# Optimization experiments

Measured on AMD Instinct MI355X. Metric: run time of the kernel, lower is better.

The kernel has to match this reference:

```python
import jax, jax.numpy as jnp
import numpy as np
from jax import lax

T, N, H, A = 128, 64, 1024, 16  # timesteps, batch(envs), hidden_size, num_actions


def _ortho(key, shape):
    # approximate nn.init.orthogonal_ via QR of a gaussian
    a = jax.random.normal(key, shape, dtype=jnp.float32)
    flip = shape[0] < shape[1]
    q, r = jnp.linalg.qr(a.T if flip else a)
    q = q * jnp.sign(jnp.diagonal(r))
    return (q.T if flip else q).astype(jnp.float32)


def setup_inputs() -> dict:
    key = jax.random.key(0)
    ks = jax.random.split(key, 10)
    c = jax.random.normal(ks[0], (T * N, H), dtype=jnp.float32)
    hxs = jax.random.normal(ks[1], (N, 2 * H), dtype=jnp.float32)
    masks = jnp.ones((T * N, 1), dtype=jnp.float32)
    prev_action_one_hot = jax.random.uniform(ks[2], (T * N, A), dtype=jnp.float32)
    # GRUCell params (torch layout: weight_ih [3H, in], weight_hh [3H, H])
    w_ih_h = _ortho(ks[3], (3 * H, H))
    w_hh_h = _ortho(ks[4], (3 * H, H))
    b_ih_h = jnp.zeros((3 * H,), dtype=jnp.float32)
    b_hh_h = jnp.zeros((3 * H,), dtype=jnp.float32)
    w_ih_p = _ortho(ks[5], (3 * H, H))
    w_hh_p = _ortho(ks[6], (3 * H, H))
    b_ih_p = jnp.zeros((3 * H,), dtype=jnp.float32)
    b_hh_p = jnp.zeros((3 * H,), dtype=jnp.float32)
    # p_network: Linear(H+A, H) -> tanh -> Linear(H, A)
    p_w1 = jax.random.normal(ks[7], (H, H + A), dtype=jnp.float32) / np.sqrt(H + A)
    p_b1 = jnp.zeros((H,), dtype=jnp.float32)
    p_w2 = jax.random.normal(ks[8], (A, H), dtype=jnp.float32) / np.sqrt(H)
    p_b2 = jnp.zeros((A,), dtype=jnp.float32)
    return dict(c=c, hxs=hxs, masks=masks, prev_action_one_hot=prev_action_one_hot,
                w_ih_h=w_ih_h, w_hh_h=w_hh_h, b_ih_h=b_ih_h, b_hh_h=b_hh_h,
                w_ih_p=w_ih_p, w_hh_p=w_hh_p, b_ih_p=b_ih_p, b_hh_p=b_hh_p,
                p_w1=p_w1, p_b1=p_b1, p_w2=p_w2, p_b2=p_b2)


def _gru_cell(x, h, w_ih, w_hh, b_ih, b_hh):
    # torch.nn.GRUCell semantics
    gi = x @ w_ih.T + b_ih  # [N, 3H]
    gh = h @ w_hh.T + b_hh  # [N, 3H]
    i_r, i_z, i_n = jnp.split(gi, 3, axis=1)
    h_r, h_z, h_n = jnp.split(gh, 3, axis=1)
    r = jax.nn.sigmoid(i_r + h_r)
    z = jax.nn.sigmoid(i_z + h_z)
    n = jnp.tanh(i_n + r * h_n)
    return (1.0 - z) * n + z * h


def reference(c, hxs, masks, prev_action_one_hot,
              w_ih_h, w_hh_h, b_ih_h, b_hh_h,
              w_ih_p, w_hh_p, b_ih_p, b_hh_p,
              p_w1, p_b1, p_w2, p_b2):
    c3 = c.reshape(T, N, H)
    m3 = masks.reshape(T, N, 1)
    a3 = prev_action_one_hot.reshape(T, N, A)
    h0 = hxs[:, :H]
    pol0 = hxs[:, H:]

    def step(carry, xs):
        h, pol = carry
        c_t, m_t, a_t = xs
        p_in = jnp.concatenate([h, a_t], axis=1) * m_t
        p_dist = jnp.tanh(p_in @ p_w1.T + p_b1) @ p_w2.T + p_b2  # [N, A]
        h = _gru_cell(c_t, h * m_t, w_ih_h, w_hh_h, b_ih_h, b_hh_h)
        pol = _gru_cell(c_t, pol * m_t, w_ih_p, w_hh_p, b_ih_p, b_hh_p)
        return (h, pol), (p_dist, pol)

    (h, pol), (acc_p_dist, acc_policy) = lax.scan(step, (h0, pol0), (c3, m3, a3))
    acc_p_dist = acc_p_dist.reshape(T * N, -1)
    acc_policy = acc_policy.reshape(T * N, -1)
    hxs_out = jnp.concatenate([h, pol], axis=1)
    return acc_p_dist, acc_policy, hxs_out
```

## Files before the change

kernel.cpp:

```cpp
#include <hip/hip_runtime.h>
#include <hip/hip_bf16.h>
#include <math.h>

#define TT 128
#define NN 64
#define HH 1024
#define AA 16
#define G3 3072
#define NC 6144
#define PK 1088
#define WLDS_STRIDE 1032
#define GISL 3072

#define PD_OFF  0
#define POL_OFF (TT*NN*AA)
#define HXS_OFF (POL_OFF + TT*NN*HH)

typedef __attribute__((ext_vector_type(8))) short short8;
typedef __attribute__((ext_vector_type(4))) float f32x4;

__device__ __align__(16) __hip_bfloat16 g_c_bf[TT*NN*HH];
__device__ __align__(16) __hip_bfloat16 g_wihc_bf[NC*HH];
__device__ __align__(16) __hip_bfloat16 g_pw1_bf[HH*PK];
__device__ __align__(16) __hip_bfloat16 g_pw2_bf[AA*HH];
__device__ float g_gi2[(size_t)2*64*TT*GISL];
__device__ float g_h[NN*HH];
__device__ float g_pol[NN*HH];
__device__ __align__(16) __hip_bfloat16 g_pin_all[(size_t)(TT+1)*NN*PK];
__device__ __align__(16) __hip_bfloat16 g_polm_all[(size_t)(TT+1)*NN*HH];
__device__ __align__(16) __hip_bfloat16 g_ph_all[TT*NN*HH];

__device__ __align__(256) unsigned g_flagsA[2][64];
__device__ __align__(256) unsigned g_gi_cnt[64];
__device__ __align__(256) unsigned g_pol_cnt[64];

__device__ __forceinline__ float sigmoidf_(float x) { return 1.0f / (1.0f + __expf(-x)); }
__device__ __forceinline__ float tanhf_(float x) {
  float e = __expf(2.0f * x);
  return 1.0f - 2.0f / (e + 1.0f);
}

__global__ __launch_bounds__(256) void conv_all(
    const float* __restrict__ c, const float* __restrict__ masks, const float* __restrict__ act,
    const float* __restrict__ wih_h, const float* __restrict__ wih_p,
    const float* __restrict__ pw1, const float* __restrict__ pw2)
{
  size_t i = (size_t)blockIdx.x * 256 + threadIdx.x;
  size_t stride = (size_t)gridDim.x * 256;
  for (size_t f = i; f < (size_t)TT*NN*HH; f += stride) g_c_bf[f] = __float2bfloat16(c[f]);
  for (size_t f = i; f < (size_t)G3*HH; f += stride) {
    g_wihc_bf[f]                 = __float2bfloat16(wih_h[f]);
    g_wihc_bf[(size_t)G3*HH + f] = __float2bfloat16(wih_p[f]);
  }
  for (size_t f = i; f < (size_t)HH*PK; f += stride) {
    int o = (int)(f / PK), j = (int)(f % PK);
    g_pw1_bf[f] = (j < HH + AA) ? __float2bfloat16(pw1[(size_t)o*(HH+AA) + j]) : __float2bfloat16(0.0f);
  }
  for (size_t f = i; f < (size_t)AA*HH; f += stride) g_pw2_bf[f] = __float2bfloat16(pw2[f]);
  for (size_t f = i; f < (size_t)TT*NN*(PK-HH); f += stride) {
    int row = (int)(f >> 6), j = (int)(f & 63);
    float v = (j < AA) ? act[(size_t)row*AA + j] * masks[row] : 0.0f;
    g_pin_all[(size_t)row*PK + HH + j] = __float2bfloat16(v);
  }
}

__global__ __launch_bounds__(256) void init_kernel(const float* __restrict__ hxs,
                                                   const float* __restrict__ masks) {
  int f = blockIdx.x * 256 + threadIdx.x;
  int n = f >> 10, j = f & 1023;
  float m0 = masks[n];
  float hv = hxs[n * 2 * HH + j];
  float pv = hxs[n * 2 * HH + HH + j];
  g_h[f] = hv;
  g_pol[f] = pv;
  g_pin_all[(size_t)n * PK + j]  = __float2bfloat16(hv * m0);
  g_polm_all[(size_t)n * HH + j] = __float2bfloat16(pv * m0);
  if (f < 128)
    __hip_atomic_store(&g_flagsA[f >> 6][f & 63], 0u,
                       __ATOMIC_RELAXED, __HIP_MEMORY_SCOPE_AGENT);
  if (f >= 128 && f < 192)
    __hip_atomic_store(&g_gi_cnt[f - 128], 0u,
                       __ATOMIC_RELAXED, __HIP_MEMORY_SCOPE_AGENT);
  if (f >= 192 && f < 256)
    __hip_atomic_store(&g_pol_cnt[f - 192], 0u,
                       __ATOMIC_RELAXED, __HIP_MEMORY_SCOPE_AGENT);
}

__global__ __launch_bounds__(256, 1) void fused_scan(
    const float* __restrict__ masks,
    const float* __restrict__ whh_h, const float* __restrict__ whh_p,
    const float* __restrict__ bih_h, const float* __restrict__ bhh_h,
    const float* __restrict__ bih_p, const float* __restrict__ bhh_p,
    const float* __restrict__ pb1, const float* __restrict__ pb2,
    float* __restrict__ out)
{
  extern __shared__ __align__(16) __hip_bfloat16 Dyn[];
  __shared__ float m_lds[TT * NN];
  __shared__ __align__(8) __hip_bfloat16 sL[NN * 16];
  const int tid = threadIdx.x, l = tid & 63, w = tid >> 6;

  if (blockIdx.x < 128) {
    __hip_bfloat16* Ws = Dyn;
    const int gru = blockIdx.x >> 6;
    const int idx = blockIdx.x & 63;
    const int c0  = idx * 16;
    const float* __restrict__ Wf = (gru == 0) ? whh_h : whh_p;

    for (int i = tid; i < TT * NN; i += 256) m_lds[i] = masks[i];

    for (int ch = tid; ch < 48 * 128; ch += 256) {
      int row = ch >> 7, ko = (ch & 127) * 8;
      int gate = row >> 4, j = row & 15;
      const float* s = Wf + (size_t)(gate * HH + c0 + j) * HH + ko;
      union { short8 v; __hip_bfloat16 hh[8]; } tmp;
#pragma unroll
      for (int q = 0; q < 8; ++q) tmp.hh[q] = __float2bfloat16(s[q]);
      *(short8*)(&Ws[row * WLDS_STRIDE + ko]) = tmp.v;
    }
    __syncthreads();

    const float* bi = (gru == 0) ? bih_h : bih_p;
    const float* bh = (gru == 0) ? bhh_h : bhh_p;
    const int col = c0 + (l & 15);
    const float bir = bi[col],        bhr = bh[col];
    const float biz = bi[HH + col],   bhz = bh[HH + col];
    const float bin = bi[2*HH + col], bhn = bh[2*HH + col];
    const int rowbase = w * 16 + (l >> 4) * 4;
    const int arow = w * 16 + (l & 15);
    const int lo8 = (l >> 4) * 8;
    const int jj = l & 15;

    float hst[4];
    {
      const float* st0 = (gru == 0) ? g_h : g_pol;
#pragma unroll
      for (int reg = 0; reg < 4; ++reg) hst[reg] = st0[(rowbase + reg) * HH + col];
    }

    unsigned gi_ready = 0;
    while (__hip_atomic_load(&g_gi_cnt[0], __ATOMIC_RELAXED,
                             __HIP_MEMORY_SCOPE_AGENT) < 48u) { }
    asm volatile("" ::: "memory");
    gi_ready = 1;
    const float* __restrict__ gib = g_gi2 + (size_t)(gru * 64 + idx) * TT * GISL;
    float gir[4], giz[4], gin[4];
#pragma unroll
    for (int reg = 0; reg < 4; ++reg) {
      const float* gp = gib + (size_t)(rowbase + reg) * 48;
      gir[reg] = gp[jj]; giz[reg] = gp[16 + jj]; gin[reg] = gp[32 + jj];
    }

    const int astr = (gru == 0) ? PK : HH;

    for (int t = 0; t < TT; ++t) {
      const __hip_bfloat16* __restrict__ Ab =
          (gru == 0) ? (g_pin_all + (size_t)t * NN * PK)
                     : (g_polm_all + (size_t)t * NN * HH);
      const __hip_bfloat16* __restrict__ arowp = Ab + (size_t)arow * astr + lo8;

      unsigned fv = __hip_atomic_load(&g_flagsA[gru][l], __ATOMIC_RELAXED,
                                      __HIP_MEMORY_SCOPE_AGENT);
      unsigned long long rdy = __ballot(fv >= (unsigned)t);
      short8 av[32];
#pragma unroll
      for (int g = 0; g < 8; ++g) {
        while (((rdy >> (g * 8)) & 0xFFull) != 0xFFull) {
          fv = __hip_atomic_load(&g_flagsA[gru][l], __ATOMIC_RELAXED,
                                 __HIP_MEMORY_SCOPE_AGENT);
          rdy = __ballot(fv >= (unsigned)t);
        }
        asm volatile("" ::: "memory");
#pragma unroll
        for (int q = 0; q < 4; ++q)
          av[g * 4 + q] = *(const short8*)(arowp + (g * 4 + q) * 32);
      }

      f32x4 acc0 = {}, acc1 = {}, acc2 = {};
#pragma unroll
      for (int u = 0; u < 32; ++u) {
        short8 b0  = *(const short8*)(&Ws[( 0 + jj) * WLDS_STRIDE + u * 32 + lo8]);
        short8 b1  = *(const short8*)(&Ws[(16 + jj) * WLDS_STRIDE + u * 32 + lo8]);
        short8 bn2 = *(const short8*)(&Ws[(32 + jj) * WLDS_STRIDE + u * 32 + lo8]);
        acc0 = __builtin_amdgcn_mfma_f32_16x16x32_bf16(av[u], b0,  acc0, 0, 0, 0);
        acc1 = __builtin_amdgcn_mfma_f32_16x16x32_bf16(av[u], b1,  acc1, 0, 0, 0);
        acc2 = __builtin_amdgcn_mfma_f32_16x16x32_bf16(av[u], bn2, acc2, 0, 0, 0);
      }

      float hv_out[4];
#pragma unroll
      for (int reg = 0; reg < 4; ++reg) {
        int row = rowbase + reg;
        float mk  = m_lds[t * NN + row];
        float mk1 = (t < TT - 1) ? m_lds[(t + 1) * NN + row] : 1.0f;
        float hm = hst[reg] * mk;
        float rg  = sigmoidf_(gir[reg] + acc0[reg] + bir + bhr);
        float z   = sigmoidf_(giz[reg] + acc1[reg] + biz + bhz);
        float nn2 = tanhf_  (gin[reg] + bin + rg * (acc2[reg] + bhn));
        float hv = (1.0f - z) * nn2 + z * hm;
        hst[reg] = hv;
        hv_out[reg] = hv;
        sL[row * 16 + jj] = __float2bfloat16(hv * mk1);
      }

      __syncthreads();
      {
        int rr = tid >> 2, cc = tid & 3;
        unsigned long long v = *(const unsigned long long*)(&sL[rr * 16 + cc * 4]);
        __hip_bfloat16* dstp = (gru == 0)
            ? (g_pin_all + (size_t)(t + 1) * NN * PK + (size_t)rr * PK + c0 + cc * 4)
            : (g_polm_all + (size_t)(t + 1) * NN * HH + (size_t)rr * HH + c0 + cc * 4);
        __hip_atomic_store((unsigned long long*)dstp, v,
                           __ATOMIC_RELAXED, __HIP_MEMORY_SCOPE_AGENT);
      }
      asm volatile("s_waitcnt vmcnt(0)" ::: "memory");
      __syncthreads();

      if (t < TT - 1) {
        if (tid == 0)
          __hip_atomic_store((unsigned*)&g_flagsA[gru][idx], (unsigned)(t + 1),
                             __ATOMIC_RELAXED, __HIP_MEMORY_SCOPE_AGENT);
        if (gru == 1) {
#pragma unroll
          for (int reg = 0; reg < 4; ++reg)
            out[POL_OFF + (size_t)(t * NN + rowbase + reg) * HH + col] = hv_out[reg];
        }
        {
          const unsigned slab = (unsigned)((t + 1) >> 1);
          if (slab >= gi_ready) {
            while (__hip_atomic_load(&g_gi_cnt[slab], __ATOMIC_RELAXED,
                                     __HIP_MEMORY_SCOPE_AGENT) < 48u) { }
            asm volatile("" ::: "memory");
            gi_ready = slab + 1;
          }
          const float* gpt = gib + (size_t)(t + 1) * GISL;
#pragma unroll
          for (int reg = 0; reg < 4; ++reg) {
            const float* gp = gpt + (size_t)(rowbase + reg) * 48;
            gir[reg] = gp[jj]; giz[reg] = gp[16 + jj]; gin[reg] = gp[32 + jj];
          }
        }
      } else {
        if (gru == 1) {
#pragma unroll
          for (int reg = 0; reg < 4; ++reg)
            out[POL_OFF + (size_t)(t * NN + rowbase + reg) * HH + col] = hv_out[reg];
        }
      }
    }

    float* stf = (gru == 0) ? g_h : g_pol;
#pragma unroll
    for (int reg = 0; reg < 4; ++reg) stf[(rowbase + reg) * HH + col] = hst[reg];

  } else {
    __hip_bfloat16* AsD = Dyn;
    __hip_bfloat16* BsD = Dyn + 2 * 128 * 72;
    const int roff = (w >> 1) * 64, coff = (w & 1) * 64;
    const int pid = blockIdx.x - 128;

    for (int kt2 = 0; kt2 < 24; ++kt2) {
      const int tile = pid + (kt2 << 7);
      const int bm = tile / 48, bn = tile % 48;
      const __hip_bfloat16* A = g_c_bf    + (size_t)bm * 128 * HH;
      const __hip_bfloat16* B = g_wihc_bf + (size_t)bn * 128 * HH;

      short8 ra[4], rb[4];
#define PG_LOAD(KT, AP, BP, STR) { _Pragma("unroll") for (int q = 0; q < 4; ++q) { \
    int cch = q * 256 + tid; int row = cch >> 3, ko = (cch & 7) * 8; \
    ra[q] = *(const short8*)((AP) + (size_t)row * (STR) + (KT) * 64 + ko); \
    rb[q] = *(const short8*)((BP) + (size_t)row * (STR) + (KT) * 64 + ko); } }
#define PG_STORE(BUF) { _Pragma("unroll") for (int q = 0; q < 4; ++q) { \
    int cch = q * 256 + tid; int row = cch >> 3, ko = (cch & 7) * 8; \
    *(short8*)(AsD + (BUF) * 9216 + row * 72 + ko) = ra[q]; \
    *(short8*)(BsD + (BUF) * 9216 + row * 72 + ko) = rb[q]; } }
#define PG_MMA(BUF) { _Pragma("unroll") for (int ks = 0; ks < 2; ++ks) { \
      short8 a[4], b[4]; \
      _Pragma("unroll") for (int fr = 0; fr < 4; ++fr) \
        a[fr] = *(const short8*)(AsD + (BUF) * 9216 + (roff + fr * 16 + (l & 15)) * 72 + ks * 32 + (l >> 4) * 8); \
      _Pragma("unroll") for (int fc = 0; fc < 4; ++fc) \
        b[fc] = *(const short8*)(BsD + (BUF) * 9216 + (coff + fc * 16 + (l & 15)) * 72 + ks * 32 + (l >> 4) * 8); \
      _Pragma("unroll") for (int fr = 0; fr < 4; ++fr) \
        _Pragma("unroll") for (int fc = 0; fc < 4; ++fc) \
          acc[fr][fc] = __builtin_amdgcn_mfma_f32_16x16x32_bf16(a[fr], b[fc], acc[fr][fc], 0, 0, 0); } }

      __syncthreads();
      PG_LOAD(0, A, B, HH) PG_STORE(0)
      f32x4 acc[4][4] = {};
      for (int kt = 0; kt < 16; ++kt) {
        __syncthreads();
        if (kt < 15) PG_LOAD(kt + 1, A, B, HH)
        PG_MMA(kt & 1)
        if (kt < 15) PG_STORE((kt + 1) & 1)
      }
#pragma unroll
      for (int fr = 0; fr < 4; ++fr)
#pragma unroll
        for (int fc = 0; fc < 4; ++fc) {
          int colg = bn * 128 + coff + fc * 16 + (l & 15);
          int q2 = colg >> 10;
          int gru2 = (q2 >= 3), gate = q2 - 3 * gru2;
          int hcol = colg & 1023, cb = hcol >> 4, j = hcol & 15;
#pragma unroll
          for (int reg = 0; reg < 4; ++reg) {
            int grow = bm * 128 + roff + fr * 16 + (l >> 4) * 4 + reg;
            int tt2 = grow >> 6, n = grow & 63;
            __hip_atomic_store(
                &g_gi2[((size_t)(gru2 * 64 + cb) * TT + tt2) * GISL + n * 48 + gate * 16 + j],
                acc[fr][fc][reg], __ATOMIC_RELAXED, __HIP_MEMORY_SCOPE_AGENT);
          }
        }
      asm volatile("s_waitcnt vmcnt(0)" ::: "memory");
      __syncthreads();
      if (tid == 0)
        __hip_atomic_fetch_add(&g_gi_cnt[bm], 1u,
                               __ATOMIC_RELAXED, __HIP_MEMORY_SCOPE_AGENT);
    }

    for (int k2 = 0; k2 < 4; ++k2) {
      const int tile = (k2 << 7) + pid;
      const int bm = tile >> 3, bn = tile & 7;
      const unsigned need = (unsigned)(2 * bm + 1);
      {
        unsigned fv;
        do {
          fv = __hip_atomic_load(&g_flagsA[0][l], __ATOMIC_RELAXED,
                                 __HIP_MEMORY_SCOPE_AGENT);
        } while (!__all(fv >= need));
        asm volatile("" ::: "memory");
      }
      const __hip_bfloat16* A = g_pin_all + (size_t)bm * 128 * PK;
      const __hip_bfloat16* B = g_pw1_bf  + (size_t)bn * 128 * PK;

      short8 ra[4], rb[4];
      __syncthreads();
      PG_LOAD(0, A, B, PK) PG_STORE(0)
      f32x4 acc[4][4] = {};
      for (int kt = 0; kt < 17; ++kt) {
        __syncthreads();
        if (kt < 16) PG_LOAD(kt + 1, A, B, PK)
        PG_MMA(kt & 1)
        if (kt < 16) PG_STORE((kt + 1) & 1)
      }
#pragma unroll
      for (int fc = 0; fc < 4; ++fc) {
        int colg = bn * 128 + coff + fc * 16 + (l & 15);
        float b1v = pb1[colg];
#pragma unroll
        for (int fr = 0; fr < 4; ++fr)
#pragma unroll
          for (int reg = 0; reg < 4; ++reg) {
            int row = bm * 128 + roff + fr * 16 + (l >> 4) * 4 + reg;
            __hip_bfloat16 hb = __float2bfloat16(tanhf_(acc[fr][fc][reg] + b1v));
            __hip_atomic_store((unsigned short*)&g_ph_all[(size_t)row * HH + colg],
                               *(unsigned short*)&hb,
                               __ATOMIC_RELAXED, __HIP_MEMORY_SCOPE_AGENT);
          }
      }
      asm volatile("s_waitcnt vmcnt(0)" ::: "memory");
      __syncthreads();
      if (tid == 0)
        __hip_atomic_fetch_add(&g_pol_cnt[bm], 1u,
                               __ATOMIC_RELAXED, __HIP_MEMORY_SCOPE_AGENT);
    }

    {
      const int r0 = pid * 64;
      const int bm2 = pid >> 1;
      while (__hip_atomic_load(&g_pol_cnt[bm2], __ATOMIC_RELAXED,
                               __HIP_MEMORY_SCOPE_AGENT) < 8u) { }
      asm volatile("" ::: "memory");
      f32x4 pa = {};
      const __hip_bfloat16* PH = g_ph_all + (size_t)(r0 + w * 16 + (l & 15)) * HH;
      const __hip_bfloat16* B  = g_pw2_bf + (size_t)(l & 15) * HH;
#pragma unroll 4
      for (int k32 = 0; k32 < 32; ++k32) {
        short8 a = *(const short8*)(PH + k32 * 32 + (l >> 4) * 8);
        short8 b = *(const short8*)(B  + k32 * 32 + (l >> 4) * 8);
        pa = __builtin_amdgcn_mfma_f32_16x16x32_bf16(a, b, pa, 0, 0, 0);
      }
      int o = l & 15;
      float bb = pb2[o];
#pragma unroll
      for (int reg = 0; reg < 4; ++reg) {
        int row = r0 + w * 16 + (l >> 4) * 4 + reg;
        out[PD_OFF + (size_t)row * AA + o] = pa[reg] + bb;
      }
    }
  }
}

__global__ __launch_bounds__(256) void final_kernel(float* __restrict__ out) {
  int f = blockIdx.x * 256 + threadIdx.x;
  int n = f >> 11, j = f & 2047;
  out[HXS_OFF + f] = (j < HH) ? g_h[n * HH + j] : g_pol[n * HH + (j - HH)];
}

extern "C" void kernel_launch(void* const* d_in, const int* in_sizes, int n_in,
                              void* d_out, int out_size, void* d_ws, size_t ws_size,
                              hipStream_t stream) {
  const float* c     = (const float*)d_in[0];
  const float* hxs   = (const float*)d_in[1];
  const float* masks = (const float*)d_in[2];
  const float* act   = (const float*)d_in[3];
  const float* wih_h = (const float*)d_in[4];
  const float* whh_h = (const float*)d_in[5];
  const float* bih_h = (const float*)d_in[6];
  const float* bhh_h = (const float*)d_in[7];
  const float* wih_p = (const float*)d_in[8];
  const float* whh_p = (const float*)d_in[9];
  const float* bih_p = (const float*)d_in[10];
  const float* bhh_p = (const float*)d_in[11];
  const float* pw1   = (const float*)d_in[12];
  const float* pb1   = (const float*)d_in[13];
  const float* pw2   = (const float*)d_in[14];
  const float* pb2   = (const float*)d_in[15];
  float* out = (float*)d_out;

  const int dyn_bytes = 48 * WLDS_STRIDE * 2;
  (void)hipFuncSetAttribute((const void*)fused_scan,
                            hipFuncAttributeMaxDynamicSharedMemorySize, dyn_bytes);

  conv_all<<<4096, 256, 0, stream>>>(c, masks, act, wih_h, wih_p, pw1, pw2);
  init_kernel<<<256, 256, 0, stream>>>(hxs, masks);
  fused_scan<<<256, 256, dyn_bytes, stream>>>(masks, whh_h, whh_p,
                                              bih_h, bhh_h, bih_p, bhh_p,
                                              pb1, pb2, out);
  final_kernel<<<512, 256, 0, stream>>>(out);
}
```

Measured before the change: 1.067 ms.

## Interleave A-row loads with MFMA and publish hidden state via direct stores

The recurrent GRU step no longer loads all 32 A fragments before running the MFMA chain. It now issues the MFMAs for each group of four fragments as soon as that group's readiness flags are observed, so waiting on other blocks overlaps with compute and fewer registers are live. The LDS staging buffer and the extra __syncthreads used to pack hidden-state outputs into 8-byte stores are removed; each thread instead writes 2-byte bf16 atomic stores straight to global memory, and the policy output store is moved into the same loop. This cuts one barrier and the LDS round-trip from the serial critical path, at the cost of many more, smaller global stores before the flag release.

```diff
diff --git a/kernel.cpp b/kernel.cpp
--- a/kernel.cpp
+++ b/kernel.cpp
@@ -96,7 +96,6 @@
 {
   extern __shared__ __align__(16) __hip_bfloat16 Dyn[];
   __shared__ float m_lds[TT * NN];
-  __shared__ __align__(8) __hip_bfloat16 sL[NN * 16];
   const int tid = threadIdx.x, l = tid & 63, w = tid >> 6;
 
   if (blockIdx.x < 128) {
@@ -161,7 +160,7 @@
       unsigned fv = __hip_atomic_load(&g_flagsA[gru][l], __ATOMIC_RELAXED,
                                       __HIP_MEMORY_SCOPE_AGENT);
       unsigned long long rdy = __ballot(fv >= (unsigned)t);
-      short8 av[32];
+      f32x4 acc0 = {}, acc1 = {}, acc2 = {};
 #pragma unroll
       for (int g = 0; g < 8; ++g) {
         while (((rdy >> (g * 8)) & 0xFFull) != 0xFFull) {
@@ -170,23 +169,22 @@
           rdy = __ballot(fv >= (unsigned)t);
         }
         asm volatile("" ::: "memory");
+        short8 av4[4];
 #pragma unroll
         for (int q = 0; q < 4; ++q)
-          av[g * 4 + q] = *(const short8*)(arowp + (g * 4 + q) * 32);
-      }
-
-      f32x4 acc0 = {}, acc1 = {}, acc2 = {};
-#pragma unroll
-      for (int u = 0; u < 32; ++u) {
-        short8 b0  = *(const short8*)(&Ws[( 0 + jj) * WLDS_STRIDE + u * 32 + lo8]);
-        short8 b1  = *(const short8*)(&Ws[(16 + jj) * WLDS_STRIDE + u * 32 + lo8]);
-        short8 bn2 = *(const short8*)(&Ws[(32 + jj) * WLDS_STRIDE + u * 32 + lo8]);
-        acc0 = __builtin_amdgcn_mfma_f32_16x16x32_bf16(av[u], b0,  acc0, 0, 0, 0);
-        acc1 = __builtin_amdgcn_mfma_f32_16x16x32_bf16(av[u], b1,  acc1, 0, 0, 0);
-        acc2 = __builtin_amdgcn_mfma_f32_16x16x32_bf16(av[u], bn2, acc2, 0, 0, 0);
-      }
-
-      float hv_out[4];
+          av4[q] = *(const short8*)(arowp + (g * 4 + q) * 32);
+#pragma unroll
+        for (int q = 0; q < 4; ++q) {
+          const int u = g * 4 + q;
+          short8 b0  = *(const short8*)(&Ws[( 0 + jj) * WLDS_STRIDE + u * 32 + lo8]);
+          short8 b1  = *(const short8*)(&Ws[(16 + jj) * WLDS_STRIDE + u * 32 + lo8]);
+          short8 bn2 = *(const short8*)(&Ws[(32 + jj) * WLDS_STRIDE + u * 32 + lo8]);
+          acc0 = __builtin_amdgcn_mfma_f32_16x16x32_bf16(av4[q], b0,  acc0, 0, 0, 0);
+          acc1 = __builtin_amdgcn_mfma_f32_16x16x32_bf16(av4[q], b1,  acc1, 0, 0, 0);
+          acc2 = __builtin_amdgcn_mfma_f32_16x16x32_bf16(av4[q], bn2, acc2, 0, 0, 0);
+        }
+      }
+
 #pragma unroll
       for (int reg = 0; reg < 4; ++reg) {
         int row = rowbase + reg;
@@ -198,32 +196,23 @@
         float nn2 = tanhf_  (gin[reg] + bin + rg * (acc2[reg] + bhn));
         float hv = (1.0f - z) * nn2 + z * hm;
         hst[reg] = hv;
-        hv_out[reg] = hv;
-        sL[row * 16 + jj] = __float2bfloat16(hv * mk1);
-      }
-
-      __syncthreads();
-      {
-        int rr = tid >> 2, cc = tid & 3;
-        unsigned long long v = *(const unsigned long long*)(&sL[rr * 16 + cc * 4]);
-        __hip_bfloat16* dstp = (gru == 0)
-            ? (g_pin_all + (size_t)(t + 1) * NN * PK + (size_t)rr * PK + c0 + cc * 4)
-            : (g_polm_all + (size_t)(t + 1) * NN * HH + (size_t)rr * HH + c0 + cc * 4);
-        __hip_atomic_store((unsigned long long*)dstp, v,
-                           __ATOMIC_RELAXED, __HIP_MEMORY_SCOPE_AGENT);
-      }
-      asm volatile("s_waitcnt vmcnt(0)" ::: "memory");
-      __syncthreads();
+        if (gru == 1) out[POL_OFF + (size_t)(t * NN + row) * HH + col] = hv;
+        if (t < TT - 1) {
+          __hip_bfloat16 hb = __float2bfloat16(hv * mk1);
+          unsigned short us; __builtin_memcpy(&us, &hb, 2);
+          unsigned short* dstp = (gru == 0)
+              ? (unsigned short*)(g_pin_all + (size_t)(t + 1) * NN * PK + (size_t)row * PK + col)
+              : (unsigned short*)(g_polm_all + (size_t)(t + 1) * NN * HH + (size_t)row * HH + col);
+          __hip_atomic_store(dstp, us, __ATOMIC_RELAXED, __HIP_MEMORY_SCOPE_AGENT);
+        }
+      }
 
       if (t < TT - 1) {
+        asm volatile("s_waitcnt vmcnt(0)" ::: "memory");
+        __syncthreads();
         if (tid == 0)
           __hip_atomic_store((unsigned*)&g_flagsA[gru][idx], (unsigned)(t + 1),
                              __ATOMIC_RELAXED, __HIP_MEMORY_SCOPE_AGENT);
-        if (gru == 1) {
-#pragma unroll
-          for (int reg = 0; reg < 4; ++reg)
-            out[POL_OFF + (size_t)(t * NN + rowbase + reg) * HH + col] = hv_out[reg];
-        }
         {
           const unsigned slab = (unsigned)((t + 1) >> 1);
           if (slab >= gi_ready) {
@@ -238,12 +227,6 @@
             const float* gp = gpt + (size_t)(rowbase + reg) * 48;
             gir[reg] = gp[jj]; giz[reg] = gp[16 + jj]; gin[reg] = gp[32 + jj];
           }
-        }
-      } else {
-        if (gru == 1) {
-#pragma unroll
-          for (int reg = 0; reg < 4; ++reg)
-            out[POL_OFF + (size_t)(t * NN + rowbase + reg) * HH + col] = hv_out[reg];
         }
       }
     }
@@ -351,8 +334,8 @@
           for (int reg = 0; reg < 4; ++reg) {
             int row = bm * 128 + roff + fr * 16 + (l >> 4) * 4 + reg;
             __hip_bfloat16 hb = __float2bfloat16(tanhf_(acc[fr][fc][reg] + b1v));
-            __hip_atomic_store((unsigned short*)&g_ph_all[(size_t)row * HH + colg],
-                               *(unsigned short*)&hb,
+            unsigned short us; __builtin_memcpy(&us, &hb, 2);
+            __hip_atomic_store((unsigned short*)&g_ph_all[(size_t)row * HH + colg], us,
                                __ATOMIC_RELAXED, __HIP_MEMORY_SCOPE_AGENT);
           }
       }
```

Result: slower. 1.367 ms (+28.1%).
